# Optimization experiments

Measured on AMD Instinct MI355X. Metric: run time of the kernel, lower is better.

## Reference

```python
import jax, jax.numpy as jnp
import numpy as np

B, D, N = 16, 512, 8192
K = 2048  # codebook_size


def setup_inputs() -> dict:
    key = jax.random.key(0)
    k1, k2 = jax.random.split(key)
    x = jax.random.normal(k1, (B, D, N), dtype=jnp.float32)
    embed = jax.random.normal(k2, (K, D), dtype=jnp.float32)  # codebook [K, D]
    return {"x": x, "embed": embed}


def reference(x, embed):
    # x: [B, D, N] -> [B, N, D] -> flatten to [B*N, D]
    xt = jnp.transpose(x, (0, 2, 1))
    flat = xt.reshape(-1, xt.shape[-1])  # [B*N, D]
    x2 = jnp.sum(flat * flat, axis=1, keepdims=True)            # [B*N, 1]
    e2 = jnp.sum(embed * embed, axis=1)[None, :]                 # [1, K]
    dist = -(x2 - 2.0 * (flat @ embed.T) + e2)                   # [B*N, K]
    embed_ind = jnp.argmax(dist, axis=-1)                        # [B*N]
    embed_ind = embed_ind.reshape(B, N)                          # [B, N]
    quantize = embed[embed_ind]                                  # [B, N, D]
    quantize = jnp.transpose(quantize, (0, 2, 1))                # [B, D, N]
    return (quantize, embed_ind)
```

## Files before the change

kernel.cpp:

```cpp
#include <hip/hip_runtime.h>
#include <math.h>
#include <stdint.h>


constexpr int B = 16, D = 512, N = 8192, K = 2048;

typedef __attribute__((ext_vector_type(8)))  short   short8;
typedef __attribute__((ext_vector_type(16))) float   floatx16;

typedef const __attribute__((address_space(1))) uint32_t* gas1_t;
typedef __attribute__((address_space(3)))       uint32_t* las3_t;

__device__ __forceinline__ void async_ld16(const void* g, void* lds) {
  __builtin_amdgcn_global_load_lds((gas1_t)g, (las3_t)lds, 16, 0, 0);
}

__device__ __forceinline__ uint32_t rne_hi(float a) {
  uint32_t u = __float_as_uint(a);
  return (u + 0x7fffu + ((u >> 16) & 1u)) & 0xffff0000u;
}

__device__ __forceinline__ void split2(float a, float b, uint32_t& hi, uint32_t& lo) {
  uint32_t ha = rne_hi(a), hb = rne_hi(b);
  float ra = a - __uint_as_float(ha);
  float rb = b - __uint_as_float(hb);
  hi = (ha >> 16) | hb;
  uint32_t la = rne_hi(ra), lb = rne_hi(rb);
  lo = (la >> 16) | lb;
}

__global__ __launch_bounds__(256) void e2_kernel(const float* __restrict__ embed,
                                                 float* __restrict__ e2) {
  int k = blockIdx.x * 4 + (threadIdx.x >> 6);
  int lane = threadIdx.x & 63;
  const float* row = embed + (size_t)k * D;
  float s = 0.f;
  #pragma unroll
  for (int d = 0; d < D; d += 64) {
    float v = row[d + lane];
    s = fmaf(v, v, s);
  }
  #pragma unroll
  for (int off = 32; off; off >>= 1) s += __shfl_down(s, off, 64);
  if (lane == 0) e2[k] = s;
}

__global__ __launch_bounds__(256) void split_x(const float* __restrict__ x,
                                               ushort* __restrict__ xh,
                                               ushort* __restrict__ xl) {
  const int t  = threadIdx.x;
  const int n0 = blockIdx.x * 1024 + t * 4;
  const int g  = blockIdx.y;
  const int b  = blockIdx.z;
  const float* src = x + ((size_t)b * D + g * 8) * N + n0;
  union { ushort u[8]; short8 s; } H[4], L[4];
  #pragma unroll
  for (int r = 0; r < 8; ++r) {
    const float4 v = *(const float4*)(src + (size_t)r * N);
    const float a0 = v.x, a1 = v.y, a2 = v.z, a3 = v.w;
    uint32_t h; float res;
    h = rne_hi(a0); res = a0 - __uint_as_float(h); H[0].u[r] = (ushort)(h >> 16); L[0].u[r] = (ushort)(rne_hi(res) >> 16);
    h = rne_hi(a1); res = a1 - __uint_as_float(h); H[1].u[r] = (ushort)(h >> 16); L[1].u[r] = (ushort)(rne_hi(res) >> 16);
    h = rne_hi(a2); res = a2 - __uint_as_float(h); H[2].u[r] = (ushort)(h >> 16); L[2].u[r] = (ushort)(rne_hi(res) >> 16);
    h = rne_hi(a3); res = a3 - __uint_as_float(h); H[3].u[r] = (ushort)(h >> 16); L[3].u[r] = (ushort)(rne_hi(res) >> 16);
  }
  const size_t base = ((size_t)(b * 32 + (n0 >> 8)) * 16 + (g >> 2)) * 8192
                    + ((size_t)(g & 3) * 256 + (n0 & 255)) * 8;
  #pragma unroll
  for (int j = 0; j < 4; ++j) {
    *(short8*)&xh[base + j * 8] = H[j].s;
    *(short8*)&xl[base + j * 8] = L[j].s;
  }
}

__global__ __launch_bounds__(256) void split_e(const float* __restrict__ embed,
                                               ushort* __restrict__ eh,
                                               ushort* __restrict__ el) {
  const int t = threadIdx.x;
  const int c = blockIdx.x * 16 + (t >> 4);
  const int kt2 = c >> 8, cl = c & 255;
  #pragma unroll
  for (int p = 0; p < 8; ++p) {
    int d0 = p * 64 + (t & 15) * 4;
    const float4 v = *(const float4*)(embed + (size_t)c * D + d0);
    uint32_t h0, l0, h1, l1;
    split2(v.x, v.y, h0, l0);
    split2(v.z, v.w, h1, l1);
    int dt2 = d0 >> 5, run = (d0 >> 3) & 3, e = d0 & 7;
    size_t off = (size_t)(kt2 * 16 + dt2) * 8192 + ((size_t)run * 256 + cl) * 8 + e;
    *(uint2*)&eh[off] = make_uint2(h0, h1);
    *(uint2*)&el[off] = make_uint2(l0, l1);
  }
}

__global__ __launch_bounds__(512, 2) void vq_mfma4(const ushort* __restrict__ xh,
                                                   const ushort* __restrict__ xl,
                                                   const ushort* __restrict__ eh,
                                                   const ushort* __restrict__ el,
                                                   const float* __restrict__ e2g,
                                                   const float* __restrict__ embed,
                                                   float* __restrict__ out) {
  __shared__ ushort Xh[2][8192], Xl[2][8192];
  __shared__ ushort Eh[2][8192], El[2][8192];
  __shared__ float redV[1024];
  __shared__ int   redI[1024];
  __shared__ int   fIdx[256];

  const int t    = threadIdx.x;
  const int lane = t & 63;
  const int wid  = t >> 6;
  const int wm   = wid & 1;
  const int wn   = wid >> 1;
  const int l31  = lane & 31;
  const int lh   = lane >> 5;

  const int b  = blockIdx.y;
  const int nb = blockIdx.x;
  const int n0 = nb * 256;

  const size_t xbase = (size_t)(b * 32 + nb) * 16 * 8192;

  float bestV[2] = {-3.402823466e38f, -3.402823466e38f};
  int   bestI[2] = {0, 0};

  floatx16 acc[4][2];
  #pragma unroll
  for (int mt = 0; mt < 4; ++mt)
    #pragma unroll
    for (int nt = 0; nt < 2; ++nt)
      #pragma unroll
      for (int i = 0; i < 16; ++i) acc[mt][nt][i] = 0.f;

  auto STAGE = [&](int s, int buf) {
    const int kt2 = s >> 4, dt2 = s & 15;
    const size_t xo = xbase + (size_t)dt2 * 8192;
    const size_t eo = (size_t)(kt2 * 16 + dt2) * 8192;
    #pragma unroll
    for (int i = 0; i < 2; ++i) {
      const int o = (wid * 2 + i) * 512;
      async_ld16(xh + xo + o + lane * 8, &Xh[buf][o]);
      async_ld16(xl + xo + o + lane * 8, &Xl[buf][o]);
      async_ld16(eh + eo + o + lane * 8, &Eh[buf][o]);
      async_ld16(el + eo + o + lane * 8, &El[buf][o]);
    }
  };

  STAGE(0, 0);
  STAGE(1, 1);
  asm volatile("s_waitcnt vmcnt(8)" ::: "memory");
  __builtin_amdgcn_s_barrier();
  __builtin_amdgcn_sched_barrier(0);

  int cur = 0;
  for (int s = 0; s < 128; ++s) {
    #pragma unroll
    for (int ks = 0; ks < 2; ++ks) {
      const int run = ks * 2 + lh;
      short8 ah[4], al[4];
      #pragma unroll
      for (int mt = 0; mt < 4; ++mt) {
        const int eoff = (run * 256 + (wm * 128 + mt * 32 + l31)) * 8;
        ah[mt] = *(const short8*)&Eh[cur][eoff];
        al[mt] = *(const short8*)&El[cur][eoff];
      }
      short8 bh[2], bl[2];
      #pragma unroll
      for (int nt = 0; nt < 2; ++nt) {
        const int xoff = (run * 256 + (wn * 64 + nt * 32 + l31)) * 8;
        bh[nt] = *(const short8*)&Xh[cur][xoff];
        bl[nt] = *(const short8*)&Xl[cur][xoff];
      }
      __builtin_amdgcn_s_setprio(1);
      #pragma unroll
      for (int mt = 0; mt < 4; ++mt)
        #pragma unroll
        for (int nt = 0; nt < 2; ++nt) {
          acc[mt][nt] = __builtin_amdgcn_mfma_f32_32x32x16_bf16(
              ah[mt], bh[nt], acc[mt][nt], 0, 0, 0);
          acc[mt][nt] = __builtin_amdgcn_mfma_f32_32x32x16_bf16(
              ah[mt], bl[nt], acc[mt][nt], 0, 0, 0);
          acc[mt][nt] = __builtin_amdgcn_mfma_f32_32x32x16_bf16(
              al[mt], bh[nt], acc[mt][nt], 0, 0, 0);
        }
      __builtin_amdgcn_s_setprio(0);
    }

    if ((s & 15) == 15) {
      const int kt2 = s >> 4;
      #pragma unroll
      for (int mt = 0; mt < 4; ++mt) {
        #pragma unroll
        for (int r = 0; r < 16; ++r) {
          const int row  = (r & 3) + 8 * (r >> 2) + 4 * lh;
          const int code = kt2 * 256 + wm * 128 + mt * 32 + row;
          const float ek = e2g[code];
          #pragma unroll
          for (int nt = 0; nt < 2; ++nt) {
            const float sv = 2.0f * acc[mt][nt][r] - ek;
            if (sv > bestV[nt]) { bestV[nt] = sv; bestI[nt] = code; }
            acc[mt][nt][r] = 0.f;
          }
        }
      }
    }

    __builtin_amdgcn_sched_barrier(0);
    __builtin_amdgcn_s_barrier();
    __builtin_amdgcn_sched_barrier(0);

    if (s <= 125) {
      STAGE(s + 2, cur);
      asm volatile("s_waitcnt vmcnt(8)" ::: "memory");
    } else {
      asm volatile("s_waitcnt vmcnt(0)" ::: "memory");
    }

    __builtin_amdgcn_s_barrier();
    __builtin_amdgcn_sched_barrier(0);
    cur ^= 1;
  }

  __syncthreads();
  #pragma unroll
  for (int nt = 0; nt < 2; ++nt) {
    const int n = wn * 64 + nt * 32 + l31;
    const int slot = lh * 2 + wm;
    redV[n * 4 + slot] = bestV[nt];
    redI[n * 4 + slot] = bestI[nt];
  }
  __syncthreads();
  if (t < 256) {
    float bv = redV[t * 4]; int bi = redI[t * 4];
    #pragma unroll
    for (int s = 1; s < 4; ++s) {
      float v = redV[t * 4 + s]; int ii = redI[t * 4 + s];
      if (v > bv || (v == bv && ii < bi)) { bv = v; bi = ii; }
    }
    fIdx[t] = bi;
    out[(size_t)B * D * N + (size_t)b * N + n0 + t] = (float)bi;
  }
  __syncthreads();

  {
    const int n = t & 255;
    const int code = fIdx[n];
    const float* erow = embed + (size_t)code * D;
    float* ob = out + (size_t)b * D * N + n0 + n;
    for (int d = (t >> 8); d < D; d += 2) {
      ob[(size_t)d * N] = erow[d];
    }
  }
}

__global__ __launch_bounds__(256, 2) void vq_mfma(const float* __restrict__ x,
                                                  const float* __restrict__ embed,
                                                  const float* __restrict__ e2g,
                                                  float* __restrict__ out) {
  __shared__ float    Xraw[64 * 128];
  __shared__ uint16_t Ehi[128 * 64];
  __shared__ uint16_t Elo[128 * 64];

  const int t    = threadIdx.x;
  const int lane = t & 63;
  const int wid  = t >> 6;
  const int wm   = wid & 1;
  const int wn   = wid >> 1;
  const int l31  = lane & 31;
  const int lh   = lane >> 5;

  const int b  = blockIdx.y;
  const int n0 = blockIdx.x * 128;
  const float* xb = x + (size_t)b * D * N + n0;

  float bestV[2] = {-3.402823466e38f, -3.402823466e38f};
  int   bestI[2] = {0, 0};

  for (int kt = 0; kt < K / 128; ++kt) {
    floatx16 acc[2][2];
    #pragma unroll
    for (int mt = 0; mt < 2; ++mt)
      #pragma unroll
      for (int nt = 0; nt < 2; ++nt)
        #pragma unroll
        for (int i = 0; i < 16; ++i) acc[mt][nt][i] = 0.f;

    for (int dt = 0; dt < D / 64; ++dt) {
      {
        const float* g0 = xb + (size_t)(dt * 64 + wid * 16 + lh) * N + l31 * 4;
        #pragma unroll
        for (int i = 0; i < 8; ++i) {
          async_ld16(g0 + (size_t)(i * 2) * N, &Xraw[(wid * 16 + i * 2) * 128]);
        }
      }
      {
        const float* eb = embed + (size_t)(kt * 128) * D + dt * 64;
        const int f4 = t & 15;
        const int cr = t >> 4;
        #pragma unroll
        for (int p = 0; p < 8; ++p) {
          int c = p * 16 + cr;
          const float4 v = *(const float4*)(eb + (size_t)c * D + f4 * 4);
          uint32_t h0, l0, h1, l1;
          split2(v.x, v.y, h0, l0);
          split2(v.z, v.w, h1, l1);
          int run = f4 >> 1, half = f4 & 1;
          int off = ((run ^ (c & 7)) * 8 + half * 4);
          *(uint2*)&Ehi[c * 64 + off] = make_uint2(h0, h1);
          *(uint2*)&Elo[c * 64 + off] = make_uint2(l0, l1);
        }
      }
      __syncthreads();

      #pragma unroll
      for (int ks = 0; ks < 4; ++ks) {
        short8 ahi[2], alo[2];
        #pragma unroll
        for (int mt = 0; mt < 2; ++mt) {
          int c = wm * 64 + mt * 32 + l31;
          int run = ks * 2 + lh;
          int off = (run ^ (c & 7)) * 8;
          ahi[mt] = *(const short8*)&Ehi[c * 64 + off];
          alo[mt] = *(const short8*)&Elo[c * 64 + off];
        }
        short8 bhi[2], blo[2];
        #pragma unroll
        for (int nt = 0; nt < 2; ++nt) {
          int n = wn * 64 + nt * 32 + l31;
          int kb = ks * 16 + lh * 8;
          float r0 = Xraw[(kb + 0) * 128 + n];
          float r1 = Xraw[(kb + 1) * 128 + n];
          float r2 = Xraw[(kb + 2) * 128 + n];
          float r3 = Xraw[(kb + 3) * 128 + n];
          float r4 = Xraw[(kb + 4) * 128 + n];
          float r5 = Xraw[(kb + 5) * 128 + n];
          float r6 = Xraw[(kb + 6) * 128 + n];
          float r7 = Xraw[(kb + 7) * 128 + n];
          union { short8 s; uint32_t u[4]; } Bh, Bl;
          split2(r0, r1, Bh.u[0], Bl.u[0]);
          split2(r2, r3, Bh.u[1], Bl.u[1]);
          split2(r4, r5, Bh.u[2], Bl.u[2]);
          split2(r6, r7, Bh.u[3], Bl.u[3]);
          bhi[nt] = Bh.s; blo[nt] = Bl.s;
        }
        #pragma unroll
        for (int mt = 0; mt < 2; ++mt)
          #pragma unroll
          for (int nt = 0; nt < 2; ++nt) {
            acc[mt][nt] = __builtin_amdgcn_mfma_f32_32x32x16_bf16(
                ahi[mt], bhi[nt], acc[mt][nt], 0, 0, 0);
            acc[mt][nt] = __builtin_amdgcn_mfma_f32_32x32x16_bf16(
                ahi[mt], blo[nt], acc[mt][nt], 0, 0, 0);
            acc[mt][nt] = __builtin_amdgcn_mfma_f32_32x32x16_bf16(
                alo[mt], bhi[nt], acc[mt][nt], 0, 0, 0);
          }
      }
      __syncthreads();
    }

    #pragma unroll
    for (int mt = 0; mt < 2; ++mt) {
      #pragma unroll
      for (int r = 0; r < 16; ++r) {
        int row  = (r & 3) + 8 * (r >> 2) + 4 * lh;
        int code = kt * 128 + wm * 64 + mt * 32 + row;
        float ek = e2g[code];
        #pragma unroll
        for (int nt = 0; nt < 2; ++nt) {
          float s = 2.0f * acc[mt][nt][r] - ek;
          if (s > bestV[nt]) { bestV[nt] = s; bestI[nt] = code; }
        }
      }
    }
  }

  __syncthreads();
  float* redV = Xraw;
  int*   redI = (int*)(Xraw + 512);
  int*   fIdx = (int*)(Xraw + 1024);

  #pragma unroll
  for (int nt = 0; nt < 2; ++nt) {
    int n = wn * 64 + nt * 32 + l31;
    int slot = lh + 2 * wm;
    redV[n * 4 + slot] = bestV[nt];
    redI[n * 4 + slot] = bestI[nt];
  }
  __syncthreads();
  if (t < 128) {
    float bv = redV[t * 4]; int bi = redI[t * 4];
    #pragma unroll
    for (int s = 1; s < 4; ++s) {
      float v = redV[t * 4 + s]; int ii = redI[t * 4 + s];
      if (v > bv || (v == bv && ii < bi)) { bv = v; bi = ii; }
    }
    fIdx[t] = bi;
    out[(size_t)B * D * N + (size_t)b * N + n0 + t] = (float)bi;
  }
  __syncthreads();

  {
    int n = t & 127;
    int code = fIdx[n];
    const float* erow = embed + (size_t)code * D;
    float* ob = out + (size_t)b * D * N + n0 + n;
    for (int d = (t >> 7); d < D; d += 2) {
      ob[(size_t)d * N] = erow[d];
    }
  }
}

extern "C" void kernel_launch(void* const* d_in, const int* in_sizes, int n_in,
                              void* d_out, int out_size, void* d_ws, size_t ws_size,
                              hipStream_t stream) {
  const float* x     = (const float*)d_in[0];
  const float* embed = (const float*)d_in[1];
  float* out = (float*)d_out;

  const size_t ES = (size_t)K * D;
  const size_t XS = (size_t)B * D * N;
  const size_t need = 8192 + 2 * ES * 2 + 2 * XS * 2;

  float* e2 = (float*)d_ws;

  if (ws_size >= need) {
    ushort* eh = (ushort*)((char*)d_ws + 8192);
    ushort* el = eh + ES;
    ushort* xhp = el + ES;
    ushort* xlp = xhp + XS;
    e2_kernel<<<dim3(K / 4), 256, 0, stream>>>(embed, e2);
    split_e<<<dim3(K / 16), 256, 0, stream>>>(embed, eh, el);
    split_x<<<dim3(N / 1024, D / 8, B), 256, 0, stream>>>(x, xhp, xlp);
    vq_mfma4<<<dim3(N / 256, B), 512, 0, stream>>>(xhp, xlp, eh, el, e2, embed, out);
  } else {
    e2_kernel<<<dim3(K / 4), 256, 0, stream>>>(embed, e2);
    vq_mfma<<<dim3(N / 128, B), 256, 0, stream>>>(x, embed, e2, out);
  }
}
```

Measured before the change: 1.272 ms.

## Restructure VQ MFMA loop into 4-slot half-stage pipeline with split X/E prefetch

After: 1.227 ms. 1.04x faster.

```diff
diff --git a/kernel.cpp b/kernel.cpp
--- a/kernel.cpp
+++ b/kernel.cpp
@@ -93,18 +93,19 @@
   }
 }
 
-__global__ __launch_bounds__(512, 2) void vq_mfma4(const ushort* __restrict__ xh,
+__global__ __launch_bounds__(512, 2) void vq_mfma5(const ushort* __restrict__ xh,
                                                    const ushort* __restrict__ xl,
                                                    const ushort* __restrict__ eh,
                                                    const ushort* __restrict__ el,
                                                    const float* __restrict__ e2g,
                                                    const float* __restrict__ embed,
                                                    float* __restrict__ out) {
-  __shared__ ushort Xh[2][8192], Xl[2][8192];
-  __shared__ ushort Eh[2][8192], El[2][8192];
-  __shared__ float redV[1024];
-  __shared__ int   redI[1024];
-  __shared__ int   fIdx[256];
+  __shared__ ushort XhL[16384], XlL[16384];
+  __shared__ ushort EhL[16384], ElL[16384];
+  __shared__ float  e2L[2048];
+  __shared__ float  redV[1024];
+  __shared__ int    redI[1024];
+  __shared__ int    fIdx[256];
 
   const int t    = threadIdx.x;
   const int lane = t & 63;
@@ -120,6 +121,10 @@
 
   const size_t xbase = (size_t)(b * 32 + nb) * 16 * 8192;
 
+  #pragma unroll
+  for (int i = 0; i < 4; ++i) e2L[t + i * 512] = e2g[t + i * 512];
+  __syncthreads();
+
   float bestV[2] = {-3.402823466e38f, -3.402823466e38f};
   int   bestI[2] = {0, 0};
 
@@ -131,69 +136,99 @@
       #pragma unroll
       for (int i = 0; i < 16; ++i) acc[mt][nt][i] = 0.f;
 
-  auto STAGE = [&](int s, int buf) {
-    const int kt2 = s >> 4, dt2 = s & 15;
-    const size_t xo = xbase + (size_t)dt2 * 8192;
-    const size_t eo = (size_t)(kt2 * 16 + dt2) * 8192;
-    #pragma unroll
-    for (int i = 0; i < 2; ++i) {
-      const int o = (wid * 2 + i) * 512;
-      async_ld16(xh + xo + o + lane * 8, &Xh[buf][o]);
-      async_ld16(xl + xo + o + lane * 8, &Xl[buf][o]);
-      async_ld16(eh + eo + o + lane * 8, &Eh[buf][o]);
-      async_ld16(el + eo + o + lane * 8, &El[buf][o]);
-    }
+  auto STAGE_X = [&](int up) {
+    const int dt2 = (up >> 1) & 15, ks = up & 1, hb = up & 3;
+    const size_t so = xbase + (size_t)dt2 * 8192 + ks * 4096 + wid * 512 + lane * 8;
+    async_ld16(xh + so, &XhL[hb * 4096 + wid * 512]);
+    async_ld16(xl + so, &XlL[hb * 4096 + wid * 512]);
   };
-
-  STAGE(0, 0);
-  STAGE(1, 1);
+  auto STAGE_E = [&](int up) {
+    const int kt2 = up >> 5, dt2 = (up >> 1) & 15, ks = up & 1, hb = up & 3;
+    const size_t so = (size_t)(kt2 * 16 + dt2) * 8192 + ks * 4096 + wid * 512 + lane * 8;
+    async_ld16(eh + so, &EhL[hb * 4096 + wid * 512]);
+    async_ld16(el + so, &ElL[hb * 4096 + wid * 512]);
+  };
+
+  STAGE_X(0); STAGE_E(0);
+  STAGE_X(1); STAGE_E(1);
+  STAGE_X(2); STAGE_E(2);
   asm volatile("s_waitcnt vmcnt(8)" ::: "memory");
   __builtin_amdgcn_s_barrier();
   __builtin_amdgcn_sched_barrier(0);
 
-  int cur = 0;
-  for (int s = 0; s < 128; ++s) {
-    #pragma unroll
-    for (int ks = 0; ks < 2; ++ks) {
-      const int run = ks * 2 + lh;
-      short8 ah[4], al[4];
-      #pragma unroll
-      for (int mt = 0; mt < 4; ++mt) {
-        const int eoff = (run * 256 + (wm * 128 + mt * 32 + l31)) * 8;
-        ah[mt] = *(const short8*)&Eh[cur][eoff];
-        al[mt] = *(const short8*)&El[cur][eoff];
-      }
-      short8 bh[2], bl[2];
+  const int rb   = lh * 2048;
+  const int xo0  = rb + (wn * 64 + l31) * 8;
+  const int ao0  = rb + (wm * 128 + l31) * 8;
+
+  for (int u = 0; u < 256; ++u) {
+    const int hb4 = (u & 3) * 4096;
+
+    short8 bh[2], bl[2], a0h[2], a0l[2];
+    #pragma unroll
+    for (int nt = 0; nt < 2; ++nt) {
+      const int xo = hb4 + xo0 + nt * 256;
+      bh[nt] = *(const short8*)&XhL[xo];
+      bl[nt] = *(const short8*)&XlL[xo];
+    }
+    #pragma unroll
+    for (int m2 = 0; m2 < 2; ++m2) {
+      const int eo = hb4 + ao0 + m2 * 256;
+      a0h[m2] = *(const short8*)&EhL[eo];
+      a0l[m2] = *(const short8*)&ElL[eo];
+    }
+    if (u <= 252) STAGE_X(u + 3);
+    __builtin_amdgcn_s_barrier();
+    asm volatile("s_waitcnt lgkmcnt(0)" ::: "memory");
+    __builtin_amdgcn_sched_barrier(0);
+    __builtin_amdgcn_s_setprio(1);
+    #pragma unroll
+    for (int m2 = 0; m2 < 2; ++m2)
       #pragma unroll
       for (int nt = 0; nt < 2; ++nt) {
-        const int xoff = (run * 256 + (wn * 64 + nt * 32 + l31)) * 8;
-        bh[nt] = *(const short8*)&Xh[cur][xoff];
-        bl[nt] = *(const short8*)&Xl[cur][xoff];
-      }
-      __builtin_amdgcn_s_setprio(1);
-      #pragma unroll
-      for (int mt = 0; mt < 4; ++mt)
-        #pragma unroll
-        for (int nt = 0; nt < 2; ++nt) {
-          acc[mt][nt] = __builtin_amdgcn_mfma_f32_32x32x16_bf16(
-              ah[mt], bh[nt], acc[mt][nt], 0, 0, 0);
-          acc[mt][nt] = __builtin_amdgcn_mfma_f32_32x32x16_bf16(
-              ah[mt], bl[nt], acc[mt][nt], 0, 0, 0);
-          acc[mt][nt] = __builtin_amdgcn_mfma_f32_32x32x16_bf16(
-              al[mt], bh[nt], acc[mt][nt], 0, 0, 0);
-        }
-      __builtin_amdgcn_s_setprio(0);
-    }
-
-    if ((s & 15) == 15) {
-      const int kt2 = s >> 4;
+        acc[m2][nt] = __builtin_amdgcn_mfma_f32_32x32x16_bf16(
+            a0h[m2], bh[nt], acc[m2][nt], 0, 0, 0);
+        acc[m2][nt] = __builtin_amdgcn_mfma_f32_32x32x16_bf16(
+            a0h[m2], bl[nt], acc[m2][nt], 0, 0, 0);
+        acc[m2][nt] = __builtin_amdgcn_mfma_f32_32x32x16_bf16(
+            a0l[m2], bh[nt], acc[m2][nt], 0, 0, 0);
+      }
+    __builtin_amdgcn_s_setprio(0);
+    __builtin_amdgcn_s_barrier();
+
+    short8 a1h[2], a1l[2];
+    #pragma unroll
+    for (int m2 = 0; m2 < 2; ++m2) {
+      const int eo = hb4 + ao0 + (2 + m2) * 256;
+      a1h[m2] = *(const short8*)&EhL[eo];
+      a1l[m2] = *(const short8*)&ElL[eo];
+    }
+    if (u <= 252) STAGE_E(u + 3);
+    __builtin_amdgcn_s_barrier();
+    asm volatile("s_waitcnt lgkmcnt(0)" ::: "memory");
+    __builtin_amdgcn_sched_barrier(0);
+    __builtin_amdgcn_s_setprio(1);
+    #pragma unroll
+    for (int m2 = 0; m2 < 2; ++m2)
+      #pragma unroll
+      for (int nt = 0; nt < 2; ++nt) {
+        acc[2 + m2][nt] = __builtin_amdgcn_mfma_f32_32x32x16_bf16(
+            a1h[m2], bh[nt], acc[2 + m2][nt], 0, 0, 0);
+        acc[2 + m2][nt] = __builtin_amdgcn_mfma_f32_32x32x16_bf16(
+            a1h[m2], bl[nt], acc[2 + m2][nt], 0, 0, 0);
+        acc[2 + m2][nt] = __builtin_amdgcn_mfma_f32_32x32x16_bf16(
+            a1l[m2], bh[nt], acc[2 + m2][nt], 0, 0, 0);
+      }
+    __builtin_amdgcn_s_setprio(0);
+
+    if ((u & 31) == 31) {
+      const int kt2 = u >> 5;
       #pragma unroll
       for (int mt = 0; mt < 4; ++mt) {
         #pragma unroll
         for (int r = 0; r < 16; ++r) {
           const int row  = (r & 3) + 8 * (r >> 2) + 4 * lh;
           const int code = kt2 * 256 + wm * 128 + mt * 32 + row;
-          const float ek = e2g[code];
+          const float ek = e2L[code];
           #pragma unroll
           for (int nt = 0; nt < 2; ++nt) {
             const float sv = 2.0f * acc[mt][nt][r] - ek;
@@ -204,20 +239,13 @@
       }
     }
 
-    __builtin_amdgcn_sched_barrier(0);
-    __builtin_amdgcn_s_barrier();
-    __builtin_amdgcn_sched_barrier(0);
-
-    if (s <= 125) {
-      STAGE(s + 2, cur);
+    if (u <= 252) {
       asm volatile("s_waitcnt vmcnt(8)" ::: "memory");
     } else {
       asm volatile("s_waitcnt vmcnt(0)" ::: "memory");
     }
-
     __builtin_amdgcn_s_barrier();
     __builtin_amdgcn_sched_barrier(0);
-    cur ^= 1;
   }
 
   __syncthreads();
@@ -430,7 +458,7 @@
     e2_kernel<<<dim3(K / 4), 256, 0, stream>>>(embed, e2);
     split_e<<<dim3(K / 16), 256, 0, stream>>>(embed, eh, el);
     split_x<<<dim3(N / 1024, D / 8, B), 256, 0, stream>>>(x, xhp, xlp);
-    vq_mfma4<<<dim3(N / 256, B), 512, 0, stream>>>(xhp, xlp, eh, el, e2, embed, out);
+    vq_mfma5<<<dim3(N / 256, B), 512, 0, stream>>>(xhp, xlp, eh, el, e2, embed, out);
   } else {
     e2_kernel<<<dim3(K / 4), 256, 0, stream>>>(embed, e2);
     vq_mfma<<<dim3(N / 128, B), 256, 0, stream>>>(x, embed, e2, out);
```
